# Kernel tuning notes

Hardware: AMD Instinct MI355X
Metric: run time of the kernel (lower is better)

Reference implementation:

```python
import jax, jax.numpy as jnp
import numpy as np

N_NODES = 100      # fixed: actor_fc expects 6000 = 100 * 60
IN_C    = 65536    # chev_conv_state_dim
OUT_C   = 60
K       = 3        # Chebyshev order
ACTION  = 100
N_EDGES = 1600


def setup_inputs() -> dict:
    key = jax.random.key(0)
    ks = jax.random.split(key, 20)
    s = 0.02  # small init scale
    f32 = jnp.float32
    return {
        "substrate_features": jax.random.normal(ks[0], (N_NODES, IN_C), f32),
        "substrate_edge_index": jax.random.randint(ks[1], (2, N_EDGES), 0, N_NODES),
        "vnr_features": jax.random.uniform(ks[2], (1, 3), f32),
        # ChebConv params: weight [K, IN_C, OUT_C], bias [OUT_C]
        "actor_cheb_w": (jax.random.normal(ks[3], (K, IN_C, OUT_C), f32) * s),
        "actor_cheb_b": jnp.zeros((OUT_C,), f32),
        "critic_cheb_w": (jax.random.normal(ks[4], (K, IN_C, OUT_C), f32) * s),
        "critic_cheb_b": jnp.zeros((OUT_C,), f32),
        # three Linear(1,60) per head, stacked: w [3, 60], b [3, 60]
        "actor_vnr_w": jax.random.normal(ks[5], (3, OUT_C), f32) * s,
        "actor_vnr_b": jnp.zeros((3, OUT_C), f32),
        "critic_vnr_w": jax.random.normal(ks[6], (3, OUT_C), f32) * s,
        "critic_vnr_b": jnp.zeros((3, OUT_C), f32),
        # heads
        "actor_fc_w": jax.random.normal(ks[7], (N_NODES * OUT_C, ACTION), f32) * s,
        "actor_fc_b": jnp.zeros((ACTION,), f32),
        "critic_fc_w": jax.random.normal(ks[8], (N_NODES * OUT_C, 1), f32) * s,
        "critic_fc_b": jnp.zeros((1,), f32),
    }


def _cheb_conv(x, src, dst, W, b):
    """PyG ChebConv with sym normalization, lambda_max=2 => L_hat = -D^-1/2 A D^-1/2.
    Z0 = x, Z1 = L_hat x, Z2 = 2 L_hat Z1 - Z0; out = sum_k Zk @ W[k] + b."""
    n = x.shape[0]
    ones = jnp.ones(src.shape[0], x.dtype)
    deg = jax.ops.segment_sum(ones, src, num_segments=n)
    dinv = jnp.where(deg > 0, jax.lax.rsqrt(jnp.maximum(deg, 1.0)), 0.0)
    w_norm = -dinv[src] * dinv[dst]  # [E]

    def lhat(z):  # sparse propagate: gather src rows, scale, scatter-add at dst
        return jax.ops.segment_sum(w_norm[:, None] * z[src], dst, num_segments=n)

    z0 = x
    z1 = lhat(z0)
    z2 = 2.0 * lhat(z1) - z0
    return z0 @ W[0] + z1 @ W[1] + z2 @ W[2] + b


def _vnr_sum(v, w, b):
    # sum of three Linear(1,60) outputs on scalars v[0], v[1], v[2] -> [60]
    return (v[:, None] * w + b).sum(axis=0)


def reference(substrate_features, substrate_edge_index, vnr_features,
              actor_cheb_w, actor_cheb_b, critic_cheb_w, critic_cheb_b,
              actor_vnr_w, actor_vnr_b, critic_vnr_w, critic_vnr_b,
              actor_fc_w, actor_fc_b, critic_fc_w, critic_fc_b):
    src, dst = substrate_edge_index[0], substrate_edge_index[1]
    v = vnr_features[0]  # [3]

    emb_a = jnp.tanh(_cheb_conv(substrate_features, src, dst, actor_cheb_w, actor_cheb_b))
    emb_a = emb_a + _vnr_sum(v, actor_vnr_w, actor_vnr_b)  # broadcast [N,60] + [60]
    flat_a = emb_a.reshape(1, -1)  # [1, 6000]
    logits = flat_a @ actor_fc_w + actor_fc_b  # [1, ACTION]

    emb_c = jnp.tanh(_cheb_conv(substrate_features, src, dst, critic_cheb_w, critic_cheb_b))
    emb_c = emb_c + _vnr_sum(v, critic_vnr_w, critic_vnr_b)
    flat_c = emb_c.reshape(1, -1)
    values = flat_c @ critic_fc_w + critic_fc_b  # [1, 1]

    return logits, values
```

## Files before the change

### kernel.cpp

```cpp
#include <hip/hip_runtime.h>
#include <math.h>

#define KDIM    65536
#define NNODES  100
#define OUTC    60
#define YW      64
#define YSLAB   (NNODES*YW)

#define BK5     64
#define ITERS5  16
#define SLAB5   (BK5*ITERS5)
#define NKC5    (KDIM/SLAB5)
#define CHUNK   256
#define NKC     256
#define STEPS   (CHUNK/32)

#define WS_S    0
#define WS_Y    10048
#define WS_E    48448
#define XB_OFF_BYTES   245760ull
#define XB_BYTES       (100ull*65536ull*2ull)
#define WS_NEED_BYTES  (XB_OFF_BYTES + XB_BYTES)
#define YP_OFF_BYTES   WS_NEED_BYTES
#define YP_FLOATS      ((size_t)NKC5 * 6 * YSLAB)
#define WS_NEED2_BYTES (YP_OFF_BYTES + YP_FLOATS * 4ull)

typedef short bf16x8 __attribute__((ext_vector_type(8)));
typedef float f32x4  __attribute__((ext_vector_type(4)));
typedef unsigned short ushort8 __attribute__((ext_vector_type(8)));

__device__ inline unsigned short f2bf(float f) {
    union { float f; unsigned u; } x; x.f = f;
    unsigned r = x.u + 0x7FFFu + ((x.u >> 16) & 1u);
    return (unsigned short)(r >> 16);
}

__global__ __launch_bounds__(256) void k_build_s(const int* __restrict__ ei,
                                                 float* __restrict__ S) {
    __shared__ int   deg[NNODES];
    __shared__ float dinv[NNODES];
    const int t = threadIdx.x;
    if (t < NNODES) deg[t] = 0;
    __syncthreads();
    const int* src = ei;
    const int* dst = ei + 1600;
    for (int e = t; e < 1600; e += 256) atomicAdd(&deg[src[e]], 1);
    __syncthreads();
    if (t < NNODES) { int d = deg[t]; dinv[t] = (d > 0) ? rsqrtf((float)d) : 0.f; }
    __syncthreads();
    for (int e = t; e < 1600; e += 256) {
        int s = src[e], d = dst[e];
        atomicAdd(&S[d * NNODES + s], -dinv[s] * dinv[d]);
    }
}

__global__ __launch_bounds__(256) void k_cvt_x(const float* __restrict__ x,
                                               ushort8* __restrict__ xb) {
    int g = blockIdx.x * 256 + threadIdx.x;
    for (int i = g; i < 819200; i += 204800) {
        const float4 lo = ((const float4*)x)[2 * i];
        const float4 hi = ((const float4*)x)[2 * i + 1];
        ushort8 o;
        o[0] = f2bf(lo.x); o[1] = f2bf(lo.y); o[2] = f2bf(lo.z); o[3] = f2bf(lo.w);
        o[4] = f2bf(hi.x); o[5] = f2bf(hi.y); o[6] = f2bf(hi.z); o[7] = f2bf(hi.w);
        xb[i] = o;
    }
}

template <bool DIRECT>
__global__ __launch_bounds__(256) void k_gemm5(const unsigned short* __restrict__ xb,
                                               const float* __restrict__ wa,
                                               const float* __restrict__ wc,
                                               float* __restrict__ Y,
                                               float* __restrict__ Yp) {
    __shared__ unsigned short Ab[2][112 * BK5];
    __shared__ float          Wf[2][BK5 * OUTC];
    const int hk   = blockIdx.x;
    const int kc   = blockIdx.y;
    const int wave = threadIdx.x >> 6;
    const int lane = threadIdx.x & 63;
    const int n16  = lane & 15;
    const int quad = lane >> 4;
    const int c0   = wave * 16;
    const int cidx = min(c0 + n16, OUTC - 1);
    const int kb0  = kc * SLAB5;

    const float* Wg = (hk < 3 ? wa : wc) + (size_t)(hk % 3) * ((size_t)KDIM * OUTC);

    auto DMA = [&](int buf, int kb) {
        for (int j = wave; j < 14; j += 4) {
            int chunk = j * 64 + lane;
            int m  = chunk >> 3;
            int cc = (chunk & 7) ^ (m & 7);
            const unsigned short* src = xb + (size_t)min(m, NNODES - 1) * KDIM + kb + cc * 8;
            __builtin_amdgcn_global_load_lds(
                (const __attribute__((address_space(1))) void*)src,
                (__attribute__((address_space(3))) void*)&Ab[buf][j * 512], 16, 0, 0);
        }
        const float* wsrc = Wg + (size_t)kb * OUTC;
        for (int j = wave; j < 15; j += 4) {
            __builtin_amdgcn_global_load_lds(
                (const __attribute__((address_space(1))) void*)(wsrc + j * 256 + lane * 4),
                (__attribute__((address_space(3))) void*)&Wf[buf][j * 256], 16, 0, 0);
        }
    };

    DMA(0, kb0);
    f32x4 acc[7] = {};

#pragma unroll
    for (int it = 0; it < ITERS5; ++it) {
        __syncthreads();
        if (it + 1 < ITERS5) DMA((it + 1) & 1, kb0 + (it + 1) * BK5);
        const unsigned short* A = Ab[it & 1];
        const float*          B = Wf[it & 1];
#pragma unroll
        for (int s = 0; s < 2; ++s) {
            bf16x8 bfr;
#pragma unroll
            for (int j = 0; j < 8; ++j) {
                int jj = (j + quad * 2) & 7;
                bfr[jj] = (short)f2bf(B[(s * 32 + quad * 8 + jj) * OUTC + cidx]);
            }
            int ch = (s * 4 + quad) ^ (n16 & 7);
#pragma unroll
            for (int t = 0; t < 7; ++t) {
                bf16x8 afr = *(const bf16x8*)(A + (t * 16 + n16) * BK5 + ch * 8);
                acc[t] = __builtin_amdgcn_mfma_f32_16x16x32_bf16(afr, bfr, acc[t], 0, 0, 0);
            }
        }
    }

    float* Yb = DIRECT ? (Yp + ((size_t)kc * 6 + hk) * YSLAB) : (Y + hk * YSLAB);
#pragma unroll
    for (int t = 0; t < 7; ++t)
#pragma unroll
        for (int r = 0; r < 4; ++r) {
            int row = t * 16 + quad * 4 + r;
            if (row < NNODES) {
                if (DIRECT) Yb[row * YW + c0 + n16] = acc[t][r];
                else        atomicAdd(&Yb[row * YW + c0 + n16], acc[t][r]);
            }
        }
}

__global__ __launch_bounds__(256) void k_reduce(const float* __restrict__ P,
                                                float* __restrict__ Y) {
    int g = blockIdx.x * 256 + threadIdx.x;
    if (g >= 9600) return;
    const f32x4* p = (const f32x4*)P + g;
    f32x4 s = {};
#pragma unroll 4
    for (int kc = 0; kc < NKC5; ++kc) s += p[(size_t)kc * 9600];
    ((f32x4*)Y)[g] = s;
}

__global__ __launch_bounds__(256, 2) void k_gemm_f32(const float* __restrict__ x,
                                                     const float* __restrict__ wa,
                                                     const float* __restrict__ wc,
                                                     float* __restrict__ Y) {
    const int hk   = blockIdx.x;
    const int kc   = blockIdx.y;
    const int wave = threadIdx.x >> 6;
    const int lane = threadIdx.x & 63;
    const int n16  = lane & 15;
    const int quad = lane >> 4;
    const float* W = (hk < 3 ? wa : wc) + (size_t)(hk % 3) * ((size_t)KDIM * OUTC);
    const int c0   = wave * 16;
    const int cidx = min(c0 + n16, OUTC - 1);
    const int kb0  = kc * CHUNK + quad * 8;
    const float* ap[7];
#pragma unroll
    for (int t = 0; t < 7; ++t)
        ap[t] = x + (size_t)min(n16 + 16 * t, NNODES - 1) * KDIM + kb0;
    const float* bp = W + (size_t)kb0 * OUTC + cidx;
    f32x4 acc[7] = {};
#pragma unroll 2
    for (int s = 0; s < STEPS; ++s) {
        bf16x8 bfr;
        const float* q = bp + (size_t)s * 32 * OUTC;
#pragma unroll
        for (int j = 0; j < 8; ++j) bfr[j] = (short)f2bf(q[j * OUTC]);
#pragma unroll
        for (int t = 0; t < 7; ++t) {
            const float* p = ap[t] + s * 32;
            float4 lo = *(const float4*)p;
            float4 hi = *(const float4*)(p + 4);
            bf16x8 afr;
            afr[0] = (short)f2bf(lo.x); afr[1] = (short)f2bf(lo.y);
            afr[2] = (short)f2bf(lo.z); afr[3] = (short)f2bf(lo.w);
            afr[4] = (short)f2bf(hi.x); afr[5] = (short)f2bf(hi.y);
            afr[6] = (short)f2bf(hi.z); afr[7] = (short)f2bf(hi.w);
            acc[t] = __builtin_amdgcn_mfma_f32_16x16x32_bf16(afr, bfr, acc[t], 0, 0, 0);
        }
    }
    float* Yb = Y + hk * YSLAB;
#pragma unroll
    for (int t = 0; t < 7; ++t)
#pragma unroll
        for (int r = 0; r < 4; ++r) {
            int row = t * 16 + quad * 4 + r;
            if (row < NNODES)
                atomicAdd(&Yb[row * YW + c0 + n16], acc[t][r]);
        }
}

__global__ __launch_bounds__(128) void k_emb(const float* __restrict__ S,
                                             const float* __restrict__ Y,
                                             const float* __restrict__ vnr,
                                             const float* __restrict__ avw,
                                             const float* __restrict__ avb,
                                             const float* __restrict__ cvw,
                                             const float* __restrict__ cvb,
                                             const float* __restrict__ acb,
                                             const float* __restrict__ ccb,
                                             const float* __restrict__ afcb,
                                             const float* __restrict__ cfcb,
                                             float* __restrict__ E,
                                             float* __restrict__ out) {
    __shared__ float Sp[NNODES * 101];
    __shared__ float y0[NNODES], y1[NNODES], y2[NNODES], t2[NNODES];
    const int b = blockIdx.x, head = b / OUTC, c = b % OUTC;
    const int t = threadIdx.x;

    for (int i = t; i < NNODES * NNODES; i += 128)
        Sp[(i / NNODES) * 101 + (i % NNODES)] = S[i];
    const float* Yh = Y + (size_t)head * 3 * YSLAB;
    if (t < NNODES) {
        y0[t] = Yh[t * YW + c];
        y1[t] = Yh[YSLAB + t * YW + c];
        y2[t] = Yh[2 * YSLAB + t * YW + c];
    }
    if (b == 0 && t < 101) out[t] = (t < 100) ? afcb[t] : cfcb[0];
    __syncthreads();

    float z1 = 0.f, s2 = 0.f;
    if (t < NNODES) {
        const float* sr = Sp + t * 101;
        for (int m = 0; m < NNODES; ++m) { z1 += sr[m] * y1[m]; s2 += sr[m] * y2[m]; }
        t2[t] = s2;
    }
    __syncthreads();
    if (t < NNODES) {
        const float* sr = Sp + t * 101;
        float t3 = 0.f;
        for (int m = 0; m < NNODES; ++m) t3 += sr[m] * t2[m];
        const float* cb = head ? ccb : acb;
        const float* vw = head ? cvw : avw;
        const float* vb = head ? cvb : avb;
        float u  = y0[t] + z1 + 2.f * t3 - y2[t] + cb[c];
        float vs = vnr[0] * vw[c]        + vb[c]
                 + vnr[1] * vw[OUTC + c] + vb[OUTC + c]
                 + vnr[2] * vw[2*OUTC+c] + vb[2*OUTC+c];
        E[head * (NNODES * OUTC) + t * OUTC + c] = tanhf(u) + vs;
    }
}

__global__ __launch_bounds__(128) void k_heads(const float* __restrict__ E,
                                               const float* __restrict__ afw,
                                               const float* __restrict__ cfw,
                                               float* __restrict__ out) {
    __shared__ float ea[25], ec[25];
    const int b = blockIdx.x, t = threadIdx.x;
    const int f0 = b * 25;
    if (t < 25) {
        ea[t] = E[f0 + t];
        ec[t] = E[NNODES * OUTC + f0 + t];
    }
    __syncthreads();
    if (t < 100) {
        float s = 0.f;
#pragma unroll
        for (int i = 0; i < 25; ++i) s += ea[i] * afw[(size_t)(f0 + i) * 100 + t];
        atomicAdd(&out[t], s);
    } else if (t == 100) {
        float s = 0.f;
#pragma unroll
        for (int i = 0; i < 25; ++i) s += ec[i] * cfw[f0 + i];
        atomicAdd(&out[100], s);
    }
}

extern "C" void kernel_launch(void* const* d_in, const int* in_sizes, int n_in,
                              void* d_out, int out_size, void* d_ws, size_t ws_size,
                              hipStream_t stream) {
    const float* x    = (const float*)d_in[0];
    const int*   ei   = (const int*)  d_in[1];
    const float* vnr  = (const float*)d_in[2];
    const float* wa   = (const float*)d_in[3];
    const float* acb  = (const float*)d_in[4];
    const float* wc   = (const float*)d_in[5];
    const float* ccb  = (const float*)d_in[6];
    const float* avw  = (const float*)d_in[7];
    const float* avb  = (const float*)d_in[8];
    const float* cvw  = (const float*)d_in[9];
    const float* cvb  = (const float*)d_in[10];
    const float* afw  = (const float*)d_in[11];
    const float* afcb = (const float*)d_in[12];
    const float* cfw  = (const float*)d_in[13];
    const float* cfcb = (const float*)d_in[14];

    float* ws = (float*)d_ws;
    float* S  = ws + WS_S;
    float* Y  = ws + WS_Y;
    float* E  = ws + WS_E;
    float* out = (float*)d_out;

    hipMemsetAsync(ws, 0, (size_t)WS_E * sizeof(float), stream);
    k_build_s<<<1, 256, 0, stream>>>(ei, S);

    if (ws_size >= WS_NEED2_BYTES) {
        unsigned short* xb = (unsigned short*)((char*)d_ws + XB_OFF_BYTES);
        float* Yp = (float*)((char*)d_ws + YP_OFF_BYTES);
        k_cvt_x<<<800, 256, 0, stream>>>(x, (ushort8*)xb);
        k_gemm5<true><<<dim3(6, NKC5), 256, 0, stream>>>(xb, wa, wc, Y, Yp);
        k_reduce<<<38, 256, 0, stream>>>(Yp, Y);
    } else if (ws_size >= WS_NEED_BYTES) {
        unsigned short* xb = (unsigned short*)((char*)d_ws + XB_OFF_BYTES);
        k_cvt_x<<<800, 256, 0, stream>>>(x, (ushort8*)xb);
        k_gemm5<false><<<dim3(6, NKC5), 256, 0, stream>>>(xb, wa, wc, Y, nullptr);
    } else {
        k_gemm_f32<<<dim3(6, NKC), 256, 0, stream>>>(x, wa, wc, Y);
    }

    k_emb<<<120, 128, 0, stream>>>(S, Y, vnr, avw, avb, cvw, cvb,
                                   acb, ccb, afcb, cfcb, E, out);
    k_heads<<<240, 128, 0, stream>>>(E, afw, cfw, out);
}
```

Before: 214.5 us.

## Widen GEMM blocks to 8 waves with manual vmcnt pipelining; fold S build into emb

```diff
diff --git a/kernel.cpp b/kernel.cpp
--- a/kernel.cpp
+++ b/kernel.cpp
@@ -33,25 +33,6 @@
     union { float f; unsigned u; } x; x.f = f;
     unsigned r = x.u + 0x7FFFu + ((x.u >> 16) & 1u);
     return (unsigned short)(r >> 16);
-}
-
-__global__ __launch_bounds__(256) void k_build_s(const int* __restrict__ ei,
-                                                 float* __restrict__ S) {
-    __shared__ int   deg[NNODES];
-    __shared__ float dinv[NNODES];
-    const int t = threadIdx.x;
-    if (t < NNODES) deg[t] = 0;
-    __syncthreads();
-    const int* src = ei;
-    const int* dst = ei + 1600;
-    for (int e = t; e < 1600; e += 256) atomicAdd(&deg[src[e]], 1);
-    __syncthreads();
-    if (t < NNODES) { int d = deg[t]; dinv[t] = (d > 0) ? rsqrtf((float)d) : 0.f; }
-    __syncthreads();
-    for (int e = t; e < 1600; e += 256) {
-        int s = src[e], d = dst[e];
-        atomicAdd(&S[d * NNODES + s], -dinv[s] * dinv[d]);
-    }
 }
 
 __global__ __launch_bounds__(256) void k_cvt_x(const float* __restrict__ x,
@@ -68,80 +49,104 @@
 }
 
 template <bool DIRECT>
-__global__ __launch_bounds__(256) void k_gemm5(const unsigned short* __restrict__ xb,
+__global__ __launch_bounds__(512) void k_gemm6(const unsigned short* __restrict__ xb,
                                                const float* __restrict__ wa,
                                                const float* __restrict__ wc,
                                                float* __restrict__ Y,
                                                float* __restrict__ Yp) {
     __shared__ unsigned short Ab[2][112 * BK5];
-    __shared__ float          Wf[2][BK5 * OUTC];
+    __shared__ float          Wf[2][4096];
+    __shared__ float          padlds[256];
     const int hk   = blockIdx.x;
     const int kc   = blockIdx.y;
     const int wave = threadIdx.x >> 6;
     const int lane = threadIdx.x & 63;
     const int n16  = lane & 15;
     const int quad = lane >> 4;
-    const int c0   = wave * 16;
+    const int ng   = wave & 3;
+    const int mg   = wave >> 2;
+    const int c0   = ng * 16;
     const int cidx = min(c0 + n16, OUTC - 1);
+    const int NT   = 4 - mg;
     const int kb0  = kc * SLAB5;
 
     const float* Wg = (hk < 3 ? wa : wc) + (size_t)(hk % 3) * ((size_t)KDIM * OUTC);
 
     auto DMA = [&](int buf, int kb) {
-        for (int j = wave; j < 14; j += 4) {
-            int chunk = j * 64 + lane;
-            int m  = chunk >> 3;
-            int cc = (chunk & 7) ^ (m & 7);
-            const unsigned short* src = xb + (size_t)min(m, NNODES - 1) * KDIM + kb + cc * 8;
+        const float* wsrc = Wg + (size_t)kb * OUTC;
+#pragma unroll
+        for (int j5 = 0; j5 < 4; ++j5) {
+            int j = wave + j5 * 8;
+            const void* src; void* dst;
+            if (j < 16) {
+                int chunk = j * 64 + lane;
+                int m  = chunk >> 3;
+                int cc = (chunk & 7) ^ (m & 7);
+                src = xb + (size_t)min(m, NNODES - 1) * KDIM + kb + cc * 8;
+                dst = (j < 14) ? (void*)&Ab[buf][j * 512] : (void*)padlds;
+            } else {
+                int jj = j - 16;
+                src = wsrc + (jj == 15 ? 0 : jj * 256) + lane * 4;
+                dst = &Wf[buf][jj * 256];
+            }
             __builtin_amdgcn_global_load_lds(
                 (const __attribute__((address_space(1))) void*)src,
-                (__attribute__((address_space(3))) void*)&Ab[buf][j * 512], 16, 0, 0);
-        }
-        const float* wsrc = Wg + (size_t)kb * OUTC;
-        for (int j = wave; j < 15; j += 4) {
-            __builtin_amdgcn_global_load_lds(
-                (const __attribute__((address_space(1))) void*)(wsrc + j * 256 + lane * 4),
-                (__attribute__((address_space(3))) void*)&Wf[buf][j * 256], 16, 0, 0);
+                (__attribute__((address_space(3))) void*)dst, 16, 0, 0);
         }
     };
 
     DMA(0, kb0);
-    f32x4 acc[7] = {};
+    f32x4 acc[4] = {};
 
 #pragma unroll
     for (int it = 0; it < ITERS5; ++it) {
-        __syncthreads();
-        if (it + 1 < ITERS5) DMA((it + 1) & 1, kb0 + (it + 1) * BK5);
+        if (it + 1 < ITERS5) {
+            DMA((it + 1) & 1, kb0 + (it + 1) * BK5);
+            asm volatile("s_waitcnt vmcnt(4)" ::: "memory");
+        } else {
+            asm volatile("s_waitcnt vmcnt(0)" ::: "memory");
+        }
+        __builtin_amdgcn_s_barrier();
+        asm volatile("" ::: "memory");
         const unsigned short* A = Ab[it & 1];
         const float*          B = Wf[it & 1];
 #pragma unroll
         for (int s = 0; s < 2; ++s) {
             bf16x8 bfr;
 #pragma unroll
-            for (int j = 0; j < 8; ++j) {
-                int jj = (j + quad * 2) & 7;
+            for (int jq = 0; jq < 8; ++jq) {
+                int jj = (jq + quad * 2) & 7;
                 bfr[jj] = (short)f2bf(B[(s * 32 + quad * 8 + jj) * OUTC + cidx]);
             }
             int ch = (s * 4 + quad) ^ (n16 & 7);
 #pragma unroll
-            for (int t = 0; t < 7; ++t) {
-                bf16x8 afr = *(const bf16x8*)(A + (t * 16 + n16) * BK5 + ch * 8);
-                acc[t] = __builtin_amdgcn_mfma_f32_16x16x32_bf16(afr, bfr, acc[t], 0, 0, 0);
+            for (int t = 0; t < 4; ++t) {
+                if (t < NT) {
+                    int T = mg * 4 + t;
+                    bf16x8 afr = *(const bf16x8*)(A + (T * 16 + n16) * BK5 + ch * 8);
+                    acc[t] = __builtin_amdgcn_mfma_f32_16x16x32_bf16(afr, bfr, acc[t], 0, 0, 0);
+                }
             }
         }
+        asm volatile("" ::: "memory");
+        __builtin_amdgcn_s_barrier();
     }
 
     float* Yb = DIRECT ? (Yp + ((size_t)kc * 6 + hk) * YSLAB) : (Y + hk * YSLAB);
 #pragma unroll
-    for (int t = 0; t < 7; ++t)
-#pragma unroll
-        for (int r = 0; r < 4; ++r) {
-            int row = t * 16 + quad * 4 + r;
-            if (row < NNODES) {
-                if (DIRECT) Yb[row * YW + c0 + n16] = acc[t][r];
-                else        atomicAdd(&Yb[row * YW + c0 + n16], acc[t][r]);
+    for (int t = 0; t < 4; ++t) {
+        if (t < NT) {
+            int T = mg * 4 + t;
+#pragma unroll
+            for (int r = 0; r < 4; ++r) {
+                int row = T * 16 + quad * 4 + r;
+                if (row < NNODES) {
+                    if (DIRECT) Yb[row * YW + c0 + n16] = acc[t][r];
+                    else        atomicAdd(&Yb[row * YW + c0 + n16], acc[t][r]);
+                }
             }
         }
+    }
 }
 
 __global__ __launch_bounds__(256) void k_reduce(const float* __restrict__ P,
@@ -205,7 +210,7 @@
         }
 }
 
-__global__ __launch_bounds__(128) void k_emb(const float* __restrict__ S,
+__global__ __launch_bounds__(128) void k_emb(const int* __restrict__ ei,
                                              const float* __restrict__ Y,
                                              const float* __restrict__ vnr,
                                              const float* __restrict__ avw,
@@ -220,11 +225,24 @@
                                              float* __restrict__ out) {
     __shared__ float Sp[NNODES * 101];
     __shared__ float y0[NNODES], y1[NNODES], y2[NNODES], t2[NNODES];
+    __shared__ int   deg[NNODES];
+    __shared__ float dinv[NNODES];
     const int b = blockIdx.x, head = b / OUTC, c = b % OUTC;
     const int t = threadIdx.x;
-
-    for (int i = t; i < NNODES * NNODES; i += 128)
-        Sp[(i / NNODES) * 101 + (i % NNODES)] = S[i];
+    const int* src = ei;
+    const int* dst = ei + 1600;
+
+    for (int i = t; i < NNODES * 101; i += 128) Sp[i] = 0.f;
+    if (t < NNODES) deg[t] = 0;
+    __syncthreads();
+    for (int e = t; e < 1600; e += 128) atomicAdd(&deg[src[e]], 1);
+    __syncthreads();
+    if (t < NNODES) { int d = deg[t]; dinv[t] = (d > 0) ? rsqrtf((float)d) : 0.f; }
+    __syncthreads();
+    for (int e = t; e < 1600; e += 128) {
+        int s = src[e], d = dst[e];
+        atomicAdd(&Sp[d * 101 + s], -dinv[s] * dinv[d]);
+    }
     const float* Yh = Y + (size_t)head * 3 * YSLAB;
     if (t < NNODES) {
         y0[t] = Yh[t * YW + c];
@@ -301,29 +319,27 @@
     const float* cfcb = (const float*)d_in[14];
 
     float* ws = (float*)d_ws;
-    float* S  = ws + WS_S;
     float* Y  = ws + WS_Y;
     float* E  = ws + WS_E;
     float* out = (float*)d_out;
-
-    hipMemsetAsync(ws, 0, (size_t)WS_E * sizeof(float), stream);
-    k_build_s<<<1, 256, 0, stream>>>(ei, S);
 
     if (ws_size >= WS_NEED2_BYTES) {
         unsigned short* xb = (unsigned short*)((char*)d_ws + XB_OFF_BYTES);
         float* Yp = (float*)((char*)d_ws + YP_OFF_BYTES);
         k_cvt_x<<<800, 256, 0, stream>>>(x, (ushort8*)xb);
-        k_gemm5<true><<<dim3(6, NKC5), 256, 0, stream>>>(xb, wa, wc, Y, Yp);
+        k_gemm6<true><<<dim3(6, NKC5), 512, 0, stream>>>(xb, wa, wc, Y, Yp);
         k_reduce<<<38, 256, 0, stream>>>(Yp, Y);
     } else if (ws_size >= WS_NEED_BYTES) {
         unsigned short* xb = (unsigned short*)((char*)d_ws + XB_OFF_BYTES);
+        hipMemsetAsync((char*)d_ws + WS_Y * 4, 0, (WS_E - WS_Y) * 4, stream);
         k_cvt_x<<<800, 256, 0, stream>>>(x, (ushort8*)xb);
-        k_gemm5<false><<<dim3(6, NKC5), 256, 0, stream>>>(xb, wa, wc, Y, nullptr);
+        k_gemm6<false><<<dim3(6, NKC5), 512, 0, stream>>>(xb, wa, wc, Y, nullptr);
     } else {
+        hipMemsetAsync((char*)d_ws + WS_Y * 4, 0, (WS_E - WS_Y) * 4, stream);
         k_gemm_f32<<<dim3(6, NKC), 256, 0, stream>>>(x, wa, wc, Y);
     }
 
-    k_emb<<<120, 128, 0, stream>>>(S, Y, vnr, avw, avb, cvw, cvb,
+    k_emb<<<120, 128, 0, stream>>>(ei, Y, vnr, avw, avb, cvw, cvb,
                                    acb, ccb, afcb, cfcb, E, out);
     k_heads<<<240, 128, 0, stream>>>(E, afw, cfw, out);
 }
```

Result: slower. 237.4 us (+10.7%).
